# Kernel tuning notes

Hardware: AMD Instinct MI355X
Metric: run time of the kernel (lower is better)

## Reference

```python
import jax, jax.numpy as jnp
import numpy as np

B, T, L, D, H, S = 8, 8, 257, 1024, 16, 8
C = D // H


def _ln(x, g, b, axes):
    mu = jnp.mean(x, axes, keepdims=True)
    var = jnp.var(x, axes, keepdims=True)
    return (x - mu) * jax.lax.rsqrt(var + 1e-5) * g + b


def setup_inputs() -> dict:
    key = jax.random.key(0)
    ks = jax.random.split(key, 16)
    r = lambda i, shape, std=0.02: jax.random.normal(ks[i], shape, jnp.float32) * std
    return dict(
        x=r(0, (B, T, L, D), 1.0),
        s=r(1, (B, S, D), 1.0),
        te=r(2, (T, D), 1.0),
        patch_mask=jnp.zeros((B, T, 1, L - 1, 1), jnp.float32),
        in_proj_w=r(3, (3 * D, D)), in_proj_b=r(4, (3 * D,)),
        out_w=r(5, (D, D)), out_b=r(6, (D,)),
        ln1_g=jnp.ones(D), ln1_b=jnp.zeros(D),
        ln2_g=jnp.ones(D), ln2_b=jnp.zeros(D),
        fc_w=r(7, (4 * D, D)), fc_b=r(8, (4 * D,)),
        proj_w=r(9, (D, 4 * D)), proj_b=r(10, (D,)),
        smlp_ln_g=jnp.ones(D), smlp_ln_b=jnp.zeros(D),
        smlp_w1=r(11, (D // 8, D), 0.001), smlp_w2=r(12, (D, D // 8), 0.001),
        lnte_g=jnp.ones((T, D)), lnte_b=jnp.zeros((T, D)),
        conv_w=r(13, (D, 1, 3), 0.001), conv_b=jnp.zeros(D),
    )


def reference(x, s, te, patch_mask, in_proj_w, in_proj_b, out_w, out_b,
              ln1_g, ln1_b, ln2_g, ln2_b, fc_w, fc_b, proj_w, proj_b,
              smlp_ln_g, smlp_ln_b, smlp_w1, smlp_w2, lnte_g, lnte_b,
              conv_w, conv_b):
    scale = 1.0 / (C ** 0.5)

    def qkv(z):
        p = z @ in_proj_w.T + in_proj_b
        return jnp.split(p, 3, axis=-1)

    heads = lambda a: a.reshape(*a.shape[:-1], H, C)

    def mlp(z):
        h = z @ fc_w.T + fc_b
        h = h * jax.nn.sigmoid(1.702 * h)  # QuickGELU
        return h @ proj_w.T + proj_b

    # ---- spatial attention (per frame) ----
    xn = _ln(x, ln1_g, ln1_b, -1)
    q, k, v = [heads(a) for a in qkv(xn)]           # [B,T,L,H,C]
    aff = jnp.einsum('ntqhc,ntkhc->ntqkh', q * scale, k)
    aff = jax.nn.softmax(aff, axis=3)               # softmax over key dim (-2)
    mix = jnp.einsum('ntqlh,ntlhc->ntqhc', aff, v)
    out = mix.reshape(B, T, L, D) @ out_w.T + out_b

    # ---- syno-token branch ----
    s_mlp = (_ln(s, smlp_ln_g, smlp_ln_b, -1) @ smlp_w1.T) @ smlp_w2.T
    sn = _ln(s + s_mlp, ln1_g, ln1_b, -1)
    te_n = _ln(te, lnte_g, lnte_b, (-2, -1))        # LayerNorm over (frames, d)
    s_q, s_k, s_v = [heads(a) for a in qkv(sn)]     # [B,S,H,C]
    te_q, te_k, te_v = [a.reshape(T, 1, H, C) for a in qkv(te_n)]

    kk = k[:, :, 1:] + te_k                          # [B,T,L-1,H,C]
    vv = v[:, :, 1:] + te_v
    s_aff = jnp.einsum('nqhc,ntkhc->ntqkh', s_q * scale, kk) + patch_mask
    s_aff = jax.nn.softmax(s_aff, axis=3)
    s_mix = jnp.einsum('ntqlh,ntlhc->ntqhc', s_aff, vv)   # [B,T,S,H,C]

    # depthwise temporal conv over frames, with residual
    z = s_mix.transpose(0, 2, 3, 4, 1).reshape(B * S, D, T)   # [B*S, D, T]
    zc = jax.lax.conv_general_dilated(
        z, conv_w, window_strides=(1,), padding=[(1, 1)],
        dimension_numbers=('NCH', 'OIH', 'NCH'), feature_group_count=D)
    z = zc + conv_b[None, :, None] + z
    s_mix = z.reshape(B, S, H, C, T).transpose(0, 4, 1, 2, 3)  # [B,T,S,H,C]
    s_mix = s_mix.mean(axis=1)                                 # [B,S,H,C]
    s_out = s_mix.reshape(B, S, D) @ out_w.T + out_b

    # ---- residual + MLP ----
    x = x + out
    x = x + mlp(_ln(x, ln2_g, ln2_b, -1))
    s = s + s_out
    s = s + mlp(_ln(s, ln2_g, ln2_b, -1))
    return (x, s)
```

## Files before the change

kernel.cpp:

```cpp
#include <hip/hip_runtime.h>
#include <hip/hip_bf16.h>

#define BB 8
#define TT 8
#define LL 257
#define DD 1024
#define HH 16
#define CC 64
#define SS 8
#define NTOK (BB*TT*LL)
#define D3 (3*DD)
#define DFF (4*DD)
#define MMAIN 16384
#define MTAIL 64

typedef unsigned short u16;
typedef __attribute__((ext_vector_type(8))) short short8;
typedef __attribute__((ext_vector_type(4))) short short4v;
typedef __attribute__((ext_vector_type(4))) float f32x4;

__device__ __forceinline__ float us2f(u16 u) {
    return __uint_as_float(((unsigned int)u) << 16);
}
__device__ __forceinline__ u16 f2us(float f) {
    unsigned int u = __float_as_uint(f);
    unsigned int rb = ((u >> 16) & 1u) + 0x7fffu;
    return (u16)((u + rb) >> 16);
}

__device__ __forceinline__ void gload_lds16(const u16* g, u16* l) {
    __builtin_amdgcn_global_load_lds(
        (__attribute__((address_space(1))) void*)(void*)g,
        (__attribute__((address_space(3))) void*)(void*)l, 16, 0, 0);
}

__global__ __launch_bounds__(256)
void cvt_w(const float* __restrict__ in, u16* __restrict__ out, int n4)
{
    int i = blockIdx.x * 256 + threadIdx.x;
    if (i >= n4) return;
    float4 v = reinterpret_cast<const float4*>(in)[i];
    ushort4 o;
    o.x = f2us(v.x); o.y = f2us(v.y); o.z = f2us(v.z); o.w = f2us(v.w);
    reinterpret_cast<ushort4*>(out)[i] = o;
}

__global__ __launch_bounds__(256)
void ln_rows(const float* __restrict__ X, const float* __restrict__ R,
             const float* __restrict__ g, const float* __restrict__ bta,
             u16* __restrict__ out, int M)
{
    int row = blockIdx.x;
    if (row >= M) return;
    const float* x = X + (size_t)row * DD;
    const float* r = R ? R + (size_t)row * DD : nullptr;
    int t = threadIdx.x;
    float v[4]; float s1 = 0.f, s2 = 0.f;
#pragma unroll
    for (int i = 0; i < 4; ++i) {
        float val = x[t + 256 * i];
        if (r) val += r[t + 256 * i];
        v[i] = val; s1 += val; s2 += val * val;
    }
#pragma unroll
    for (int o = 32; o > 0; o >>= 1) { s1 += __shfl_xor(s1, o, 64); s2 += __shfl_xor(s2, o, 64); }
    __shared__ float red[10];
    int wid = t >> 6, lane = t & 63;
    if (lane == 0) { red[wid] = s1; red[4 + wid] = s2; }
    __syncthreads();
    if (t == 0) {
        float a = red[0] + red[1] + red[2] + red[3];
        float q = red[4] + red[5] + red[6] + red[7];
        float mu = a * (1.f / DD);
        float var = q * (1.f / DD) - mu * mu;
        red[8] = mu; red[9] = rsqrtf(var + 1e-5f);
    }
    __syncthreads();
    float mu = red[8], rs = red[9];
#pragma unroll
    for (int i = 0; i < 4; ++i) {
        int c = t + 256 * i;
        out[(size_t)row * DD + c] = f2us((v[i] - mu) * rs * g[c] + bta[c]);
    }
}

__global__ __launch_bounds__(256)
void s_prep(const float* __restrict__ s, const float* __restrict__ te,
            const float* __restrict__ smlp_g, const float* __restrict__ smlp_b,
            const float* __restrict__ ln1_g, const float* __restrict__ ln1_b,
            const float* __restrict__ lnte_g, const float* __restrict__ lnte_b,
            const u16* __restrict__ w1b, const u16* __restrict__ w2b,
            u16* __restrict__ snte)
{
    const int blk = blockIdx.x, t = threadIdx.x;
    __shared__ float red[10];
    const int wid = t >> 6, lane = t & 63;

    if (blk == 64) {
        const int NE = TT * DD;
        float s1 = 0.f, s2 = 0.f;
        for (int i = t; i < NE; i += 256) { float v = te[i]; s1 += v; s2 += v * v; }
#pragma unroll
        for (int o = 32; o > 0; o >>= 1) { s1 += __shfl_xor(s1, o, 64); s2 += __shfl_xor(s2, o, 64); }
        if (lane == 0) { red[wid] = s1; red[4 + wid] = s2; }
        __syncthreads();
        if (t == 0) {
            float a = red[0] + red[1] + red[2] + red[3];
            float q = red[4] + red[5] + red[6] + red[7];
            float mu = a / (float)NE;
            float var = q / (float)NE - mu * mu;
            red[8] = mu; red[9] = rsqrtf(var + 1e-5f);
        }
        __syncthreads();
        float mu = red[8], rs = red[9];
        for (int i = t; i < NE; i += 256)
            snte[(size_t)64 * DD + i] = f2us((te[i] - mu) * rs * lnte_g[i] + lnte_b[i]);
        return;
    }

    __shared__ float xrow[1024];
    __shared__ float h1[128];
    const float* sr = s + (size_t)blk * DD;

    float v[4]; float s1 = 0.f, s2 = 0.f;
#pragma unroll
    for (int i = 0; i < 4; ++i) {
        float val = sr[t + 256 * i];
        v[i] = val; s1 += val; s2 += val * val;
    }
#pragma unroll
    for (int o = 32; o > 0; o >>= 1) { s1 += __shfl_xor(s1, o, 64); s2 += __shfl_xor(s2, o, 64); }
    if (lane == 0) { red[wid] = s1; red[4 + wid] = s2; }
    __syncthreads();
    if (t == 0) {
        float a = red[0] + red[1] + red[2] + red[3];
        float q = red[4] + red[5] + red[6] + red[7];
        float mu = a * (1.f / DD);
        float var = q * (1.f / DD) - mu * mu;
        red[8] = mu; red[9] = rsqrtf(var + 1e-5f);
    }
    __syncthreads();
    {
        float mu = red[8], rs = red[9];
#pragma unroll
        for (int i = 0; i < 4; ++i) {
            int c = t + 256 * i;
            xrow[c] = (v[i] - mu) * rs * smlp_g[c] + smlp_b[c];
        }
    }
    __syncthreads();
    if (t < 128) {
        const u16* wr_ = w1b + (size_t)t * DD;
        float a0 = 0.f, a1 = 0.f;
        for (int k = 0; k < DD; k += 8) {
            short4v wa = *reinterpret_cast<const short4v*>(&wr_[k]);
            short4v wb = *reinterpret_cast<const short4v*>(&wr_[k + 4]);
#pragma unroll
            for (int j = 0; j < 4; ++j) {
                a0 += xrow[k + j] * us2f((u16)wa[j]);
                a1 += xrow[k + 4 + j] * us2f((u16)wb[j]);
            }
        }
        h1[t] = a0 + a1;
    }
    __syncthreads();
    float w[4]; s1 = 0.f; s2 = 0.f;
#pragma unroll
    for (int i = 0; i < 4; ++i) {
        int d = t + 256 * i;
        const u16* w2r = w2b + (size_t)d * 128;
        float a = 0.f;
        for (int k = 0; k < 128; k += 4) {
            short4v wa = *reinterpret_cast<const short4v*>(&w2r[k]);
#pragma unroll
            for (int j = 0; j < 4; ++j) a += h1[k + j] * us2f((u16)wa[j]);
        }
        float val = sr[d] + a;
        w[i] = val; s1 += val; s2 += val * val;
    }
#pragma unroll
    for (int o = 32; o > 0; o >>= 1) { s1 += __shfl_xor(s1, o, 64); s2 += __shfl_xor(s2, o, 64); }
    __syncthreads();
    if (lane == 0) { red[wid] = s1; red[4 + wid] = s2; }
    __syncthreads();
    if (t == 0) {
        float a = red[0] + red[1] + red[2] + red[3];
        float q = red[4] + red[5] + red[6] + red[7];
        float mu = a * (1.f / DD);
        float var = q * (1.f / DD) - mu * mu;
        red[8] = mu; red[9] = rsqrtf(var + 1e-5f);
    }
    __syncthreads();
    {
        float mu = red[8], rs = red[9];
#pragma unroll
        for (int i = 0; i < 4; ++i) {
            int d = t + 256 * i;
            snte[(size_t)blk * DD + d] = f2us((w[i] - mu) * rs * ln1_g[d] + ln1_b[d]);
        }
    }
}

enum { EPI_BF16 = 0, EPI_GELU = 1, EPI_RES = 2, EPI_F32 = 3 };

template<int EPI>
__global__ __launch_bounds__(512)
void gemm256(const u16* __restrict__ A, const u16* __restrict__ W,
             const float* __restrict__ bias, int M, int N, int K,
             u16* __restrict__ outB, float* __restrict__ outF,
             const float* __restrict__ res)
{
    __shared__ u16 lds[2][4][8192];
    const int tid = threadIdx.x;
    const int lane = tid & 63;
    const int wid = tid >> 6;
    const int wr = wid >> 2, wc = wid & 3;

    const int gx = gridDim.x;
    const int nwg = gx * gridDim.y;
    int bid = blockIdx.y * gx + blockIdx.x;
    int qq = nwg >> 3, rr = nwg & 7;
    int xcd = bid & 7, idx = bid >> 3;
    int nb = (xcd < rr ? xcd * (qq + 1) : rr * (qq + 1) + (xcd - rr) * qq) + idx;
    const int m0 = (nb / gx) * 256, n0 = (nb % gx) * 256;

    int u0 = tid, u1 = tid + 512;
    int g0 = u0 >> 6, kb0 = (u0 >> 4) & 3, r0 = u0 & 15;
    int g1 = u1 >> 6, kb1 = (u1 >> 4) & 3, r1 = u1 & 15;
    int ar0 = m0 + g0 * 16 + r0; if (ar0 >= M) ar0 = M - 1;
    int ar1 = m0 + g1 * 16 + r1; if (ar1 >= M) ar1 = M - 1;
    int br0 = n0 + g0 * 16 + r0;
    int br1 = n0 + g1 * 16 + r1;
    const u16* pa0 = A + (size_t)ar0 * K + kb0 * 8;
    const u16* pa1 = A + (size_t)ar1 * K + kb1 * 8;
    const u16* pb0 = W + (size_t)br0 * K + kb0 * 8;
    const u16* pb1 = W + (size_t)br1 * K + kb1 * 8;

    f32x4 acc[8][4];
#pragma unroll
    for (int i = 0; i < 8; ++i)
#pragma unroll
        for (int j = 0; j < 4; ++j)
            acc[i][j] = (f32x4){0.f, 0.f, 0.f, 0.f};

    auto stageA = [&](int kt, int s, int bf) {
        int kc = kt * 64 + s * 32;
        gload_lds16(pa0 + kc, &lds[bf][s * 2][u0 * 8]);
        gload_lds16(pa1 + kc, &lds[bf][s * 2][u1 * 8]);
    };
    auto stageB = [&](int kt, int s, int bf) {
        int kc = kt * 64 + s * 32;
        gload_lds16(pb0 + kc, &lds[bf][s * 2 + 1][u0 * 8]);
        gload_lds16(pb1 + kc, &lds[bf][s * 2 + 1][u1 * 8]);
    };

    const int nk = K >> 6;
    stageA(0, 0, 0); stageB(0, 0, 0); stageA(0, 1, 0); stageB(0, 1, 0);
    asm volatile("s_waitcnt vmcnt(4)" ::: "memory");
    __builtin_amdgcn_s_barrier();
    __builtin_amdgcn_sched_barrier(0);

    for (int t = 0; t < nk; ++t) {
        const int bf = t & 1, bn = bf ^ 1;
        const bool st = (t + 1 < nk);
        short8 aq[4], bq[4];
#pragma unroll
        for (int j = 0; j < 4; ++j)
            bq[j] = *reinterpret_cast<const short8*>(&lds[bf][1][(wc * 4 + j) * 512 + lane * 8]);
#pragma unroll
        for (int i = 0; i < 4; ++i)
            aq[i] = *reinterpret_cast<const short8*>(&lds[bf][0][(wr * 8 + i) * 512 + lane * 8]);
        if (st) stageA(t + 1, 0, bn);
        __builtin_amdgcn_s_barrier();
        __builtin_amdgcn_s_setprio(1);
#pragma unroll
        for (int i = 0; i < 4; ++i)
#pragma unroll
            for (int j = 0; j < 4; ++j)
                acc[i][j] = __builtin_amdgcn_mfma_f32_16x16x32_bf16(aq[i], bq[j], acc[i][j], 0, 0, 0);
        __builtin_amdgcn_s_setprio(0);
        __builtin_amdgcn_s_barrier();
        __builtin_amdgcn_sched_barrier(0);
#pragma unroll
        for (int i = 0; i < 4; ++i)
            aq[i] = *reinterpret_cast<const short8*>(&lds[bf][0][(wr * 8 + 4 + i) * 512 + lane * 8]);
        if (st) stageB(t + 1, 0, bn);
        __builtin_amdgcn_s_barrier();
        __builtin_amdgcn_s_setprio(1);
#pragma unroll
        for (int i = 0; i < 4; ++i)
#pragma unroll
            for (int j = 0; j < 4; ++j)
                acc[4 + i][j] = __builtin_amdgcn_mfma_f32_16x16x32_bf16(aq[i], bq[j], acc[4 + i][j], 0, 0, 0);
        __builtin_amdgcn_s_setprio(0);
        if (st) asm volatile("s_waitcnt vmcnt(4)" ::: "memory");
        else    asm volatile("s_waitcnt vmcnt(0)" ::: "memory");
        __builtin_amdgcn_s_barrier();
        __builtin_amdgcn_sched_barrier(0);
#pragma unroll
        for (int j = 0; j < 4; ++j)
            bq[j] = *reinterpret_cast<const short8*>(&lds[bf][3][(wc * 4 + j) * 512 + lane * 8]);
#pragma unroll
        for (int i = 0; i < 4; ++i)
            aq[i] = *reinterpret_cast<const short8*>(&lds[bf][2][(wr * 8 + i) * 512 + lane * 8]);
        if (st) stageA(t + 1, 1, bn);
        __builtin_amdgcn_s_barrier();
        __builtin_amdgcn_s_setprio(1);
#pragma unroll
        for (int i = 0; i < 4; ++i)
#pragma unroll
            for (int j = 0; j < 4; ++j)
                acc[i][j] = __builtin_amdgcn_mfma_f32_16x16x32_bf16(aq[i], bq[j], acc[i][j], 0, 0, 0);
        __builtin_amdgcn_s_setprio(0);
        __builtin_amdgcn_s_barrier();
        __builtin_amdgcn_sched_barrier(0);
#pragma unroll
        for (int i = 0; i < 4; ++i)
            aq[i] = *reinterpret_cast<const short8*>(&lds[bf][2][(wr * 8 + 4 + i) * 512 + lane * 8]);
        if (st) stageB(t + 1, 1, bn);
        __builtin_amdgcn_s_barrier();
        __builtin_amdgcn_s_setprio(1);
#pragma unroll
        for (int i = 0; i < 4; ++i)
#pragma unroll
            for (int j = 0; j < 4; ++j)
                acc[4 + i][j] = __builtin_amdgcn_mfma_f32_16x16x32_bf16(aq[i], bq[j], acc[4 + i][j], 0, 0, 0);
        __builtin_amdgcn_s_setprio(0);
        if (st) asm volatile("s_waitcnt vmcnt(4)" ::: "memory");
        __builtin_amdgcn_s_barrier();
        __builtin_amdgcn_sched_barrier(0);
    }

    const int cn = lane & 15, cr = (lane >> 4) * 4;
#pragma unroll
    for (int i = 0; i < 8; ++i) {
#pragma unroll
        for (int r = 0; r < 4; ++r) {
            int m = m0 + wr * 128 + i * 16 + cr + r;
            if (m >= M) continue;
#pragma unroll
            for (int j = 0; j < 4; ++j) {
                int n = n0 + wc * 64 + j * 16 + cn;
                float c = acc[i][j][r];
                if (bias) c += bias[n];
                size_t o = (size_t)m * N + n;
                if (EPI == EPI_BF16) outB[o] = f2us(c);
                else if (EPI == EPI_GELU) { float gg = c / (1.f + __expf(-1.702f * c)); outB[o] = f2us(gg); }
                else if (EPI == EPI_RES) outF[o] = res[o] + c;
                else outF[o] = c;
            }
        }
    }
}

template<int EPI>
__global__ __launch_bounds__(256)
void gemm_mfma(const u16* __restrict__ A, const u16* __restrict__ W,
               const float* __restrict__ bias, int M, int N, int K,
               u16* __restrict__ outB, float* __restrict__ outF,
               const float* __restrict__ res)
{
    __shared__ u16 Als[3][128 * 32];
    __shared__ u16 Bls[3][128 * 32];
    const int tid = threadIdx.x;
    const int lane = tid & 63;
    const int wid = tid >> 6;
    const int wm = (wid >> 1) * 64, wn = (wid & 1) * 64;

    const int gx = gridDim.x;
    const int nwg = gx * gridDim.y;
    int bid = blockIdx.y * gx + blockIdx.x;
    int qq = nwg >> 3, rr = nwg & 7;
    int xcd = bid & 7, idx = bid >> 3;
    int nb = (xcd < rr ? xcd * (qq + 1) : rr * (qq + 1) + (xcd - rr) * qq) + idx;
    const int m0 = (nb / gx) * 128, n0 = (nb % gx) * 128;

    int o0 = tid, o1 = tid + 256;
    int g0 = o0 >> 6, kb0 = (o0 >> 4) & 3, r0 = o0 & 15;
    int g1 = o1 >> 6, kb1 = (o1 >> 4) & 3, r1 = o1 & 15;
    int ar0 = m0 + g0 * 16 + r0; if (ar0 >= M) ar0 = M - 1;
    int ar1 = m0 + g1 * 16 + r1; if (ar1 >= M) ar1 = M - 1;
    int br0 = n0 + g0 * 16 + r0;
    int br1 = n0 + g1 * 16 + r1;
    const u16* a0 = A + (size_t)ar0 * K + kb0 * 8;
    const u16* a1 = A + (size_t)ar1 * K + kb1 * 8;
    const u16* b0 = W + (size_t)br0 * K + kb0 * 8;
    const u16* b1 = W + (size_t)br1 * K + kb1 * 8;

    f32x4 acc[4][4];
#pragma unroll
    for (int i = 0; i < 4; ++i)
#pragma unroll
        for (int j = 0; j < 4; ++j)
            acc[i][j] = (f32x4){0.f, 0.f, 0.f, 0.f};

    auto stage = [&](int kt, int sl) {
        int kk = kt << 5;
        gload_lds16(a0 + kk, &Als[sl][o0 * 8]);
        gload_lds16(a1 + kk, &Als[sl][o1 * 8]);
        gload_lds16(b0 + kk, &Bls[sl][o0 * 8]);
        gload_lds16(b1 + kk, &Bls[sl][o1 * 8]);
    };
    auto compute = [&](int sl) {
        short8 af[4], bfr[4];
#pragma unroll
        for (int i = 0; i < 4; ++i)
            af[i] = *reinterpret_cast<const short8*>(&Als[sl][((wm >> 4) + i) * 512 + lane * 8]);
#pragma unroll
        for (int j = 0; j < 4; ++j)
            bfr[j] = *reinterpret_cast<const short8*>(&Bls[sl][((wn >> 4) + j) * 512 + lane * 8]);
        __builtin_amdgcn_s_setprio(1);
#pragma unroll
        for (int i = 0; i < 4; ++i)
#pragma unroll
            for (int j = 0; j < 4; ++j)
                acc[i][j] = __builtin_amdgcn_mfma_f32_16x16x32_bf16(af[i], bfr[j], acc[i][j], 0, 0, 0);
        __builtin_amdgcn_s_setprio(0);
    };

    const int nk = K >> 5;
    stage(0, 0);
    stage(1, 1);
    asm volatile("s_waitcnt vmcnt(4)" ::: "memory");
    __builtin_amdgcn_s_barrier();
    __builtin_amdgcn_sched_barrier(0);

    int t = 0;
    for (; t < nk - 2; ++t) {
        stage(t + 2, (t + 2) % 3);
        compute(t % 3);
        asm volatile("s_waitcnt vmcnt(4)" ::: "memory");
        __builtin_amdgcn_s_barrier();
        __builtin_amdgcn_sched_barrier(0);
    }
    compute(t % 3);
    asm volatile("s_waitcnt vmcnt(0)" ::: "memory");
    __builtin_amdgcn_s_barrier();
    __builtin_amdgcn_sched_barrier(0);
    ++t;
    compute(t % 3);

    const int cn = lane & 15, cr = (lane >> 4) * 4;
#pragma unroll
    for (int i = 0; i < 4; ++i) {
#pragma unroll
        for (int r = 0; r < 4; ++r) {
            int m = m0 + wm + i * 16 + cr + r;
            if (m >= M) continue;
#pragma unroll
            for (int j = 0; j < 4; ++j) {
                int n = n0 + wn + j * 16 + cn;
                float c = acc[i][j][r];
                if (bias) c += bias[n];
                size_t o = (size_t)m * N + n;
                if (EPI == EPI_BF16) outB[o] = f2us(c);
                else if (EPI == EPI_GELU) { float gg = c / (1.f + __expf(-1.702f * c)); outB[o] = f2us(gg); }
                else if (EPI == EPI_RES) outF[o] = res[o] + c;
                else outF[o] = c;
            }
        }
    }
}

#define KSTR 72
#define VSTR 296
#define PSTR 40

__global__ __launch_bounds__(256)
void spatial_attn(const u16* __restrict__ qkv, u16* __restrict__ mix)
{
    const int h = blockIdx.x, bt = blockIdx.y;
    const int hoff = h * CC;
    const size_t base = (size_t)bt * LL * D3;
    __shared__ u16 Kls[257 * KSTR];
    __shared__ u16 Vt[64 * VSTR];
    __shared__ u16 Pb[4][16 * PSTR];
    const int tid = threadIdx.x, lane = tid & 63, w = tid >> 6;
    const int c15 = lane & 15, g = lane >> 4;

    for (int idx = tid; idx < 257 * 8; idx += 256) {
        int row = idx >> 3, c8 = (idx & 7) << 3;
        float4 v = *reinterpret_cast<const float4*>(&qkv[base + (size_t)row * D3 + DD + hoff + c8]);
        *reinterpret_cast<float4*>(&Kls[row * KSTR + c8]) = v;
    }
    for (int idx = tid; idx < 288 * 64; idx += 256) {
        int key = idx >> 6, c = idx & 63;
        u16 v = 0;
        if (key < 257) v = qkv[base + (size_t)key * D3 + 2 * DD + hoff + c];
        Vt[c * VSTR + key] = v;
    }
    __syncthreads();

    u16* pb = Pb[w];
    for (int qt = w; qt < 17; qt += 4) {
        int qrow = qt * 16 + c15; if (qrow > 256) qrow = 256;
        const u16* qp = &qkv[base + (size_t)qrow * D3 + hoff + g * 8];
        short8 a0 = *reinterpret_cast<const short8*>(qp);
        short8 a1 = *reinterpret_cast<const short8*>(qp + 32);

        f32x4 sc[17];
#pragma unroll
        for (int t = 0; t < 17; ++t) sc[t] = (f32x4){0.f, 0.f, 0.f, 0.f};
        __builtin_amdgcn_s_setprio(1);
#pragma unroll
        for (int t = 0; t < 17; ++t) {
            int krow = t * 16 + c15; if (krow > 256) krow = 256;
            short8 b0 = *reinterpret_cast<const short8*>(&Kls[krow * KSTR + g * 8]);
            short8 b1 = *reinterpret_cast<const short8*>(&Kls[krow * KSTR + 32 + g * 8]);
            sc[t] = __builtin_amdgcn_mfma_f32_16x16x32_bf16(a0, b0, sc[t], 0, 0, 0);
            sc[t] = __builtin_amdgcn_mfma_f32_16x16x32_bf16(a1, b1, sc[t], 0, 0, 0);
        }
        __builtin_amdgcn_s_setprio(0);

        const bool lastv = (c15 == 0);
#pragma unroll
        for (int r = 0; r < 4; ++r) {
            float mx = -1e30f;
#pragma unroll
            for (int t = 0; t < 17; ++t) {
                float v = sc[t][r] * 0.125f;
                if (t == 16 && !lastv) v = -1e30f;
                sc[t][r] = v;
                mx = fmaxf(mx, v);
            }
            mx = fmaxf(mx, __shfl_xor(mx, 1, 64));
            mx = fmaxf(mx, __shfl_xor(mx, 2, 64));
            mx = fmaxf(mx, __shfl_xor(mx, 4, 64));
            mx = fmaxf(mx, __shfl_xor(mx, 8, 64));
            float sum = 0.f;
#pragma unroll
            for (int t = 0; t < 17; ++t) { float e = __expf(sc[t][r] - mx); sc[t][r] = e; sum += e; }
            sum += __shfl_xor(sum, 1, 64);
            sum += __shfl_xor(sum, 2, 64);
            sum += __shfl_xor(sum, 4, 64);
            sum += __shfl_xor(sum, 8, 64);
            float is = 1.f / sum;
#pragma unroll
            for (int t = 0; t < 17; ++t) sc[t][r] *= is;
        }

        f32x4 oacc[4];
#pragma unroll
        for (int ct = 0; ct < 4; ++ct) oacc[ct] = (f32x4){0.f, 0.f, 0.f, 0.f};
#pragma unroll
        for (int k0 = 0; k0 < 9; ++k0) {
            const int t0 = 2 * k0, t1 = 2 * k0 + 1;
#pragma unroll
            for (int r = 0; r < 4; ++r) {
                pb[(4 * g + r) * PSTR + c15]      = f2us(sc[t0][r]);
                pb[(4 * g + r) * PSTR + 16 + c15] = (t1 < 17) ? f2us(sc[t1][r]) : (u16)0;
            }
            short8 pa = *reinterpret_cast<const short8*>(&pb[c15 * PSTR + 8 * g]);
            __builtin_amdgcn_s_setprio(1);
#pragma unroll
            for (int ct = 0; ct < 4; ++ct) {
                short8 vb = *reinterpret_cast<const short8*>(&Vt[(16 * ct + c15) * VSTR + 32 * k0 + 8 * g]);
                oacc[ct] = __builtin_amdgcn_mfma_f32_16x16x32_bf16(pa, vb, oacc[ct], 0, 0, 0);
            }
            __builtin_amdgcn_s_setprio(0);
        }

#pragma unroll
        for (int r = 0; r < 4; ++r) {
            int q = qt * 16 + 4 * g + r;
            if (q >= LL) continue;
            size_t ob = ((size_t)bt * LL + q) * DD + hoff;
#pragma unroll
            for (int ct = 0; ct < 4; ++ct)
                mix[ob + 16 * ct + c15] = f2us(oacc[ct][r]);
        }
    }
}

#define SK 68

__global__ __launch_bounds__(256)
void s_attn(const u16* __restrict__ qkv, const u16* __restrict__ snqkv,
            const u16* __restrict__ teqkv, const float* __restrict__ pmask,
            float* __restrict__ smix)
{
    const int h = blockIdx.x, bt = blockIdx.y, b = bt >> 3, t = bt & 7;
    const int hoff = h * CC;
    const int tid = threadIdx.x, lane = tid & 63, w = tid >> 6;
    __shared__ u16 Kls[256 * SK];
    __shared__ u16 Vls[256 * SK];
    __shared__ float pls[4][256];
    const size_t base = (size_t)bt * LL * D3;

    const int c8 = (tid & 7) * 8;
    const u16* tekp = &teqkv[t * D3 + DD + hoff + c8];
    const u16* tevp = &teqkv[t * D3 + 2 * DD + hoff + c8];
    float tek[8], tev[8];
#pragma unroll
    for (int j = 0; j < 8; ++j) { tek[j] = us2f(tekp[j]); tev[j] = us2f(tevp[j]); }
#pragma unroll
    for (int pass = 0; pass < 8; ++pass) {
        int key = (tid >> 3) + 32 * pass;
        const u16* kp = &qkv[base + (size_t)(key + 1) * D3 + DD + hoff + c8];
        const u16* vp = &qkv[base + (size_t)(key + 1) * D3 + 2 * DD + hoff + c8];
        short4v k0 = *reinterpret_cast<const short4v*>(kp);
        short4v k1 = *reinterpret_cast<const short4v*>(kp + 4);
        short4v v0 = *reinterpret_cast<const short4v*>(vp);
        short4v v1 = *reinterpret_cast<const short4v*>(vp + 4);
        short4v ok0, ok1, ov0, ov1;
#pragma unroll
        for (int j = 0; j < 4; ++j) {
            ok0[j] = (short)f2us(us2f((u16)k0[j]) + tek[j]);
            ok1[j] = (short)f2us(us2f((u16)k1[j]) + tek[4 + j]);
            ov0[j] = (short)f2us(us2f((u16)v0[j]) + tev[j]);
            ov1[j] = (short)f2us(us2f((u16)v1[j]) + tev[4 + j]);
        }
        *reinterpret_cast<short4v*>(&Kls[key * SK + c8]) = ok0;
        *reinterpret_cast<short4v*>(&Kls[key * SK + c8 + 4]) = ok1;
        *reinterpret_cast<short4v*>(&Vls[key * SK + c8]) = ov0;
        *reinterpret_cast<short4v*>(&Vls[key * SK + c8 + 4]) = ov1;
    }
    __syncthreads();

    const float* pm = pmask + (size_t)bt * 256;
    for (int qi = w; qi < SS; qi += 4) {
        float qc = us2f(snqkv[(size_t)(b * SS + qi) * D3 + hoff + lane]) * 0.125f;
        float sc[4] = {0.f, 0.f, 0.f, 0.f};
        for (int c = 0; c < CC; ++c) {
            float qv = __shfl(qc, c, 64);
#pragma unroll
            for (int j = 0; j < 4; ++j)
                sc[j] += qv * us2f(Kls[(lane + 64 * j) * SK + c]);
        }
#pragma unroll
        for (int j = 0; j < 4; ++j) sc[j] += pm[lane + 64 * j];
        float mx = fmaxf(fmaxf(sc[0], sc[1]), fmaxf(sc[2], sc[3]));
#pragma unroll
        for (int o = 32; o > 0; o >>= 1) mx = fmaxf(mx, __shfl_xor(mx, o, 64));
        float sum = 0.f;
#pragma unroll
        for (int j = 0; j < 4; ++j) { sc[j] = __expf(sc[j] - mx); sum += sc[j]; }
#pragma unroll
        for (int o = 32; o > 0; o >>= 1) sum += __shfl_xor(sum, o, 64);
        float inv = 1.f / sum;
#pragma unroll
        for (int j = 0; j < 4; ++j) pls[w][lane + 64 * j] = sc[j] * inv;
        float acc = 0.f;
        for (int key = 0; key < 256; ++key)
            acc += pls[w][key] * us2f(Vls[key * SK + lane]);
        smix[(((size_t)bt * SS + qi) * HH + h) * CC + lane] = acc;
    }
}

__global__ __launch_bounds__(256)
void conv_mean(const float* __restrict__ smix, const float* __restrict__ cw,
               const float* __restrict__ cb, u16* __restrict__ out)
{
    int idx = blockIdx.x * 256 + threadIdx.x;
    int d = idx & 1023;
    int bs = idx >> 10;
    int b = bs >> 3, s_ = bs & 7;
    float z[TT];
#pragma unroll
    for (int t = 0; t < TT; ++t)
        z[t] = smix[((size_t)(b * TT + t) * SS + s_) * DD + d];
    float w0 = cw[d * 3], w1 = cw[d * 3 + 1], w2 = cw[d * 3 + 2];
    float acc = 0.f;
#pragma unroll
    for (int t = 0; t < TT; ++t) {
        float zc = w1 * z[t];
        if (t > 0)      zc += w0 * z[t - 1];
        if (t < TT - 1) zc += w2 * z[t + 1];
        acc += z[t] + zc;
    }
    out[(size_t)bs * DD + d] = f2us(acc * 0.125f + cb[d]);
}

extern "C" void kernel_launch(void* const* d_in, const int* in_sizes, int n_in,
                              void* d_out, int out_size, void* d_ws, size_t ws_size,
                              hipStream_t stream)
{
    const float* x      = (const float*)d_in[0];
    const float* s      = (const float*)d_in[1];
    const float* te     = (const float*)d_in[2];
    const float* pmask  = (const float*)d_in[3];
    const float* in_w   = (const float*)d_in[4];
    const float* in_b   = (const float*)d_in[5];
    const float* out_w  = (const float*)d_in[6];
    const float* out_b  = (const float*)d_in[7];
    const float* ln1_g  = (const float*)d_in[8];
    const float* ln1_b  = (const float*)d_in[9];
    const float* ln2_g  = (const float*)d_in[10];
    const float* ln2_b  = (const float*)d_in[11];
    const float* fc_w   = (const float*)d_in[12];
    const float* fc_b   = (const float*)d_in[13];
    const float* proj_w = (const float*)d_in[14];
    const float* proj_b = (const float*)d_in[15];
    const float* smlp_g = (const float*)d_in[16];
    const float* smlp_b = (const float*)d_in[17];
    const float* w1     = (const float*)d_in[18];
    const float* w2     = (const float*)d_in[19];
    const float* lnte_g = (const float*)d_in[20];
    const float* lnte_b = (const float*)d_in[21];
    const float* conv_w = (const float*)d_in[22];
    const float* conv_b = (const float*)d_in[23];

    float* outx = (float*)d_out;
    float* outs = outx + (size_t)NTOK * DD;

    char* ws = (char*)d_ws;
    u16* qkv    = (u16*)ws;
    u16* mixb   = (u16*)(ws + (size_t)NTOK * D3 * 2);
    u16* hidden = qkv;
    u16* xn     = (u16*)(ws + (size_t)NTOK * DFF * 2);
    char* sm    = ws + (size_t)NTOK * DFF * 2 + (size_t)NTOK * DD * 2;
    u16*  snte   = (u16*)sm;  sm += (size_t)72 * DD * 2;
    u16*  sqkv72 = (u16*)sm;  sm += (size_t)72 * D3 * 2;
    float* smix = (float*)sm; sm += (size_t)BB * TT * SS * DD * 4;
    u16*  smm   = (u16*)sm;   sm += 64 * DD * 2;
    u16*  ln2s  = (u16*)sm;   sm += 64 * DD * 2;
    u16*  hids  = (u16*)sm;   sm += 64 * DFF * 2;
    u16* in_wb   = (u16*)sm;  sm += (size_t)D3 * DD * 2;
    u16* out_wb  = (u16*)sm;  sm += (size_t)DD * DD * 2;
    u16* fc_wb   = (u16*)sm;  sm += (size_t)DFF * DD * 2;
    u16* proj_wb = (u16*)sm;  sm += (size_t)DD * DFF * 2;
    u16* w1b     = (u16*)sm;  sm += (size_t)128 * DD * 2;
    u16* w2b     = (u16*)sm;  sm += (size_t)DD * 128 * 2;

    const float* FNULL = nullptr;
    u16* UNULL = nullptr;

    auto cvt = [&](const float* src, u16* dst, int n) {
        hipLaunchKernelGGL(cvt_w, dim3((n / 4 + 255) / 256), dim3(256), 0, stream, src, dst, n / 4);
    };
    cvt(in_w,   in_wb,   D3 * DD);
    cvt(out_w,  out_wb,  DD * DD);
    cvt(fc_w,   fc_wb,   DFF * DD);
    cvt(proj_w, proj_wb, DD * DFF);
    cvt(w1,     w1b,     128 * DD);
    cvt(w2,     w2b,     DD * 128);

    const int MT64 = MMAIN / 256;

    hipLaunchKernelGGL(ln_rows, dim3(NTOK), dim3(256), 0, stream, x, FNULL, ln1_g, ln1_b, xn, NTOK);
    hipLaunchKernelGGL((gemm256<EPI_BF16>), dim3(D3 / 256, MT64), dim3(512), 0, stream,
                       xn, in_wb, in_b, MMAIN, D3, DD, qkv, (float*)nullptr, FNULL);
    hipLaunchKernelGGL((gemm_mfma<EPI_BF16>), dim3(D3 / 128, 1), dim3(256), 0, stream,
                       xn + (size_t)MMAIN * DD, in_wb, in_b, MTAIL, D3, DD,
                       qkv + (size_t)MMAIN * D3, (float*)nullptr, FNULL);
    hipLaunchKernelGGL(spatial_attn, dim3(HH, BB * TT), dim3(256), 0, stream, qkv, mixb);
    hipLaunchKernelGGL((gemm256<EPI_RES>), dim3(DD / 256, MT64), dim3(512), 0, stream,
                       mixb, out_wb, out_b, MMAIN, DD, DD, UNULL, outx, x);
    hipLaunchKernelGGL((gemm_mfma<EPI_RES>), dim3(DD / 128, 1), dim3(256), 0, stream,
                       mixb + (size_t)MMAIN * DD, out_wb, out_b, MTAIL, DD, DD,
                       UNULL, outx + (size_t)MMAIN * DD, x + (size_t)MMAIN * DD);
    hipLaunchKernelGGL(s_prep, dim3(65), dim3(256), 0, stream,
                       s, te, smlp_g, smlp_b, ln1_g, ln1_b, lnte_g, lnte_b, w1b, w2b, snte);
    hipLaunchKernelGGL((gemm_mfma<EPI_BF16>), dim3(D3 / 128, 1), dim3(256), 0, stream,
                       snte, in_wb, in_b, 72, D3, DD, sqkv72, (float*)nullptr, FNULL);
    hipLaunchKernelGGL(s_attn, dim3(HH, BB * TT), dim3(256), 0, stream,
                       qkv, sqkv72, sqkv72 + (size_t)64 * D3, pmask, smix);
    hipLaunchKernelGGL(conv_mean, dim3(256), dim3(256), 0, stream, smix, conv_w, conv_b, smm);
    hipLaunchKernelGGL((gemm_mfma<EPI_RES>), dim3(DD / 128, 1), dim3(256), 0, stream,
                       smm, out_wb, out_b, 64, DD, DD, UNULL, outs, s);
    hipLaunchKernelGGL(ln_rows, dim3(NTOK), dim3(256), 0, stream, outx, FNULL, ln2_g, ln2_b, xn, NTOK);
    hipLaunchKernelGGL((gemm256<EPI_GELU>), dim3(DFF / 256, MT64), dim3(512), 0, stream,
                       xn, fc_wb, fc_b, MMAIN, DFF, DD, hidden, (float*)nullptr, FNULL);
    hipLaunchKernelGGL((gemm_mfma<EPI_GELU>), dim3(DFF / 128, 1), dim3(256), 0, stream,
                       xn + (size_t)MMAIN * DD, fc_wb, fc_b, MTAIL, DFF, DD,
                       hidden + (size_t)MMAIN * DFF, (float*)nullptr, FNULL);
    hipLaunchKernelGGL((gemm256<EPI_RES>), dim3(DD / 256, MT64), dim3(512), 0, stream,
                       hidden, proj_wb, proj_b, MMAIN, DD, DFF, UNULL, outx, outx);
    hipLaunchKernelGGL((gemm_mfma<EPI_RES>), dim3(DD / 128, 1), dim3(256), 0, stream,
                       hidden + (size_t)MMAIN * DFF, proj_wb, proj_b, MTAIL, DD, DFF,
                       UNULL, outx + (size_t)MMAIN * DD, outx + (size_t)MMAIN * DD);
    hipLaunchKernelGGL(ln_rows, dim3(64), dim3(256), 0, stream, outs, FNULL, ln2_g, ln2_b, ln2s, 64);
    hipLaunchKernelGGL((gemm_mfma<EPI_GELU>), dim3(DFF / 128, 1), dim3(256), 0, stream,
                       ln2s, fc_wb, fc_b, 64, DFF, DD, hids, (float*)nullptr, FNULL);
    hipLaunchKernelGGL((gemm_mfma<EPI_RES>), dim3(DD / 128, 1), dim3(256), 0, stream,
                       hids, proj_wb, proj_b, 64, DD, DFF, UNULL, outs, outs);
}
```

Measured before the change: 1.426 ms.

## Replace 256x256 GEMM plus tail kernel with single 128x128 GEMM kernel

The 512-thread 256x256-tile GEMM and the separate 3-stage 128x128 tail GEMM are replaced by one 256-thread 128x128-tile kernel derived from the large one. Every projection now runs as a single launch covering all rows, which drops the tail launches. The smaller tile halves per-block reuse of A and W loads and raises global and LDS traffic per flop. In exchange it uses less LDS per block, so more blocks can be resident. The vmcnt(4) waits were kept while each k-step now issues both A and B loads together, so the wait accounting may be wrong.

```diff
diff --git a/kernel.cpp b/kernel.cpp
--- a/kernel.cpp
+++ b/kernel.cpp
@@ -11,8 +11,6 @@
 #define NTOK (BB*TT*LL)
 #define D3 (3*DD)
 #define DFF (4*DD)
-#define MMAIN 16384
-#define MTAIL 64
 
 typedef unsigned short u16;
 typedef __attribute__((ext_vector_type(8))) short short8;
@@ -204,17 +202,17 @@
 enum { EPI_BF16 = 0, EPI_GELU = 1, EPI_RES = 2, EPI_F32 = 3 };
 
 template<int EPI>
-__global__ __launch_bounds__(512)
-void gemm256(const u16* __restrict__ A, const u16* __restrict__ W,
+__global__ __launch_bounds__(256)
+void gemm128(const u16* __restrict__ A, const u16* __restrict__ W,
              const float* __restrict__ bias, int M, int N, int K,
              u16* __restrict__ outB, float* __restrict__ outF,
              const float* __restrict__ res)
 {
-    __shared__ u16 lds[2][4][8192];
+    __shared__ u16 lds[2][4][4096];
     const int tid = threadIdx.x;
     const int lane = tid & 63;
     const int wid = tid >> 6;
-    const int wr = wid >> 2, wc = wid & 3;
+    const int wr = wid >> 1, wc = wid & 1;
 
     const int gx = gridDim.x;
     const int nwg = gx * gridDim.y;
@@ -222,9 +220,9 @@
     int qq = nwg >> 3, rr = nwg & 7;
     int xcd = bid & 7, idx = bid >> 3;
     int nb = (xcd < rr ? xcd * (qq + 1) : rr * (qq + 1) + (xcd - rr) * qq) + idx;
-    const int m0 = (nb / gx) * 256, n0 = (nb % gx) * 256;
-
-    int u0 = tid, u1 = tid + 512;
+    const int m0 = (nb / gx) * 128, n0 = (nb % gx) * 128;
+
+    int u0 = tid, u1 = tid + 256;
     int g0 = u0 >> 6, kb0 = (u0 >> 4) & 3, r0 = u0 & 15;
     int g1 = u1 >> 6, kb1 = (u1 >> 4) & 3, r1 = u1 & 15;
     int ar0 = m0 + g0 * 16 + r0; if (ar0 >= M) ar0 = M - 1;
@@ -236,9 +234,9 @@
     const u16* pb0 = W + (size_t)br0 * K + kb0 * 8;
     const u16* pb1 = W + (size_t)br1 * K + kb1 * 8;
 
-    f32x4 acc[8][4];
-#pragma unroll
-    for (int i = 0; i < 8; ++i)
+    f32x4 acc[4][4];
+#pragma unroll
+    for (int i = 0; i < 4; ++i)
 #pragma unroll
         for (int j = 0; j < 4; ++j)
             acc[i][j] = (f32x4){0.f, 0.f, 0.f, 0.f};
@@ -266,11 +264,11 @@
         short8 aq[4], bq[4];
 #pragma unroll
         for (int j = 0; j < 4; ++j)
-            bq[j] = *reinterpret_cast<const short8*>(&lds[bf][1][(wc * 4 + j) * 512 + lane * 8]);
+            bq[j] = *reinterpret_cast<const short8*>(&lds[bf][1][((wc * 4 + j) * 64 + lane) * 8]);
 #pragma unroll
         for (int i = 0; i < 4; ++i)
-            aq[i] = *reinterpret_cast<const short8*>(&lds[bf][0][(wr * 8 + i) * 512 + lane * 8]);
-        if (st) stageA(t + 1, 0, bn);
+            aq[i] = *reinterpret_cast<const short8*>(&lds[bf][0][((wr * 4 + i) * 64 + lane) * 8]);
+        if (st) { stageA(t + 1, 0, bn); stageB(t + 1, 0, bn); }
         __builtin_amdgcn_s_barrier();
         __builtin_amdgcn_s_setprio(1);
 #pragma unroll
@@ -278,20 +276,6 @@
 #pragma unroll
             for (int j = 0; j < 4; ++j)
                 acc[i][j] = __builtin_amdgcn_mfma_f32_16x16x32_bf16(aq[i], bq[j], acc[i][j], 0, 0, 0);
-        __builtin_amdgcn_s_setprio(0);
-        __builtin_amdgcn_s_barrier();
-        __builtin_amdgcn_sched_barrier(0);
-#pragma unroll
-        for (int i = 0; i < 4; ++i)
-            aq[i] = *reinterpret_cast<const short8*>(&lds[bf][0][(wr * 8 + 4 + i) * 512 + lane * 8]);
-        if (st) stageB(t + 1, 0, bn);
-        __builtin_amdgcn_s_barrier();
-        __builtin_amdgcn_s_setprio(1);
-#pragma unroll
-        for (int i = 0; i < 4; ++i)
-#pragma unroll
-            for (int j = 0; j < 4; ++j)
-                acc[4 + i][j] = __builtin_amdgcn_mfma_f32_16x16x32_bf16(aq[i], bq[j], acc[4 + i][j], 0, 0, 0);
         __builtin_amdgcn_s_setprio(0);
         if (st) asm volatile("s_waitcnt vmcnt(4)" ::: "memory");
         else    asm volatile("s_waitcnt vmcnt(0)" ::: "memory");
@@ -299,11 +283,11 @@
         __builtin_amdgcn_sched_barrier(0);
 #pragma unroll
         for (int j = 0; j < 4; ++j)
-            bq[j] = *reinterpret_cast<const short8*>(&lds[bf][3][(wc * 4 + j) * 512 + lane * 8]);
+            bq[j] = *reinterpret_cast<const short8*>(&lds[bf][3][((wc * 4 + j) * 64 + lane) * 8]);
 #pragma unroll
         for (int i = 0; i < 4; ++i)
-            aq[i] = *reinterpret_cast<const short8*>(&lds[bf][2][(wr * 8 + i) * 512 + lane * 8]);
-        if (st) stageA(t + 1, 1, bn);
+            aq[i] = *reinterpret_cast<const short8*>(&lds[bf][2][((wr * 4 + i) * 64 + lane) * 8]);
+        if (st) { stageA(t + 1, 1, bn); stageB(t + 1, 1, bn); }
         __builtin_amdgcn_s_barrier();
         __builtin_amdgcn_s_setprio(1);
 #pragma unroll
@@ -311,20 +295,6 @@
 #pragma unroll
             for (int j = 0; j < 4; ++j)
                 acc[i][j] = __builtin_amdgcn_mfma_f32_16x16x32_bf16(aq[i], bq[j], acc[i][j], 0, 0, 0);
-        __builtin_amdgcn_s_setprio(0);
-        __builtin_amdgcn_s_barrier();
-        __builtin_amdgcn_sched_barrier(0);
-#pragma unroll
-        for (int i = 0; i < 4; ++i)
-            aq[i] = *reinterpret_cast<const short8*>(&lds[bf][2][(wr * 8 + 4 + i) * 512 + lane * 8]);
-        if (st) stageB(t + 1, 1, bn);
-        __builtin_amdgcn_s_barrier();
-        __builtin_amdgcn_s_setprio(1);
-#pragma unroll
-        for (int i = 0; i < 4; ++i)
-#pragma unroll
-            for (int j = 0; j < 4; ++j)
-                acc[4 + i][j] = __builtin_amdgcn_mfma_f32_16x16x32_bf16(aq[i], bq[j], acc[4 + i][j], 0, 0, 0);
         __builtin_amdgcn_s_setprio(0);
         if (st) asm volatile("s_waitcnt vmcnt(4)" ::: "memory");
         __builtin_amdgcn_s_barrier();
@@ -333,123 +303,14 @@
 
     const int cn = lane & 15, cr = (lane >> 4) * 4;
 #pragma unroll
-    for (int i = 0; i < 8; ++i) {
+    for (int i = 0; i < 4; ++i) {
 #pragma unroll
         for (int r = 0; r < 4; ++r) {
-            int m = m0 + wr * 128 + i * 16 + cr + r;
+            int m = m0 + wr * 64 + i * 16 + cr + r;
             if (m >= M) continue;
 #pragma unroll
             for (int j = 0; j < 4; ++j) {
                 int n = n0 + wc * 64 + j * 16 + cn;
-                float c = acc[i][j][r];
-                if (bias) c += bias[n];
-                size_t o = (size_t)m * N + n;
-                if (EPI == EPI_BF16) outB[o] = f2us(c);
-                else if (EPI == EPI_GELU) { float gg = c / (1.f + __expf(-1.702f * c)); outB[o] = f2us(gg); }
-                else if (EPI == EPI_RES) outF[o] = res[o] + c;
-                else outF[o] = c;
-            }
-        }
-    }
-}
-
-template<int EPI>
-__global__ __launch_bounds__(256)
-void gemm_mfma(const u16* __restrict__ A, const u16* __restrict__ W,
-               const float* __restrict__ bias, int M, int N, int K,
-               u16* __restrict__ outB, float* __restrict__ outF,
-               const float* __restrict__ res)
-{
-    __shared__ u16 Als[3][128 * 32];
-    __shared__ u16 Bls[3][128 * 32];
-    const int tid = threadIdx.x;
-    const int lane = tid & 63;
-    const int wid = tid >> 6;
-    const int wm = (wid >> 1) * 64, wn = (wid & 1) * 64;
-
-    const int gx = gridDim.x;
-    const int nwg = gx * gridDim.y;
-    int bid = blockIdx.y * gx + blockIdx.x;
-    int qq = nwg >> 3, rr = nwg & 7;
-    int xcd = bid & 7, idx = bid >> 3;
-    int nb = (xcd < rr ? xcd * (qq + 1) : rr * (qq + 1) + (xcd - rr) * qq) + idx;
-    const int m0 = (nb / gx) * 128, n0 = (nb % gx) * 128;
-
-    int o0 = tid, o1 = tid + 256;
-    int g0 = o0 >> 6, kb0 = (o0 >> 4) & 3, r0 = o0 & 15;
-    int g1 = o1 >> 6, kb1 = (o1 >> 4) & 3, r1 = o1 & 15;
-    int ar0 = m0 + g0 * 16 + r0; if (ar0 >= M) ar0 = M - 1;
-    int ar1 = m0 + g1 * 16 + r1; if (ar1 >= M) ar1 = M - 1;
-    int br0 = n0 + g0 * 16 + r0;
-    int br1 = n0 + g1 * 16 + r1;
-    const u16* a0 = A + (size_t)ar0 * K + kb0 * 8;
-    const u16* a1 = A + (size_t)ar1 * K + kb1 * 8;
-    const u16* b0 = W + (size_t)br0 * K + kb0 * 8;
-    const u16* b1 = W + (size_t)br1 * K + kb1 * 8;
-
-    f32x4 acc[4][4];
-#pragma unroll
-    for (int i = 0; i < 4; ++i)
-#pragma unroll
-        for (int j = 0; j < 4; ++j)
-            acc[i][j] = (f32x4){0.f, 0.f, 0.f, 0.f};
-
-    auto stage = [&](int kt, int sl) {
-        int kk = kt << 5;
-        gload_lds16(a0 + kk, &Als[sl][o0 * 8]);
-        gload_lds16(a1 + kk, &Als[sl][o1 * 8]);
-        gload_lds16(b0 + kk, &Bls[sl][o0 * 8]);
-        gload_lds16(b1 + kk, &Bls[sl][o1 * 8]);
-    };
-    auto compute = [&](int sl) {
-        short8 af[4], bfr[4];
-#pragma unroll
-        for (int i = 0; i < 4; ++i)
-            af[i] = *reinterpret_cast<const short8*>(&Als[sl][((wm >> 4) + i) * 512 + lane * 8]);
-#pragma unroll
-        for (int j = 0; j < 4; ++j)
-            bfr[j] = *reinterpret_cast<const short8*>(&Bls[sl][((wn >> 4) + j) * 512 + lane * 8]);
-        __builtin_amdgcn_s_setprio(1);
-#pragma unroll
-        for (int i = 0; i < 4; ++i)
-#pragma unroll
-            for (int j = 0; j < 4; ++j)
-                acc[i][j] = __builtin_amdgcn_mfma_f32_16x16x32_bf16(af[i], bfr[j], acc[i][j], 0, 0, 0);
-        __builtin_amdgcn_s_setprio(0);
-    };
-
-    const int nk = K >> 5;
-    stage(0, 0);
-    stage(1, 1);
-    asm volatile("s_waitcnt vmcnt(4)" ::: "memory");
-    __builtin_amdgcn_s_barrier();
-    __builtin_amdgcn_sched_barrier(0);
-
-    int t = 0;
-    for (; t < nk - 2; ++t) {
-        stage(t + 2, (t + 2) % 3);
-        compute(t % 3);
-        asm volatile("s_waitcnt vmcnt(4)" ::: "memory");
-        __builtin_amdgcn_s_barrier();
-        __builtin_amdgcn_sched_barrier(0);
-    }
-    compute(t % 3);
-    asm volatile("s_waitcnt vmcnt(0)" ::: "memory");
-    __builtin_amdgcn_s_barrier();
-    __builtin_amdgcn_sched_barrier(0);
-    ++t;
-    compute(t % 3);
-
-    const int cn = lane & 15, cr = (lane >> 4) * 4;
-#pragma unroll
-    for (int i = 0; i < 4; ++i) {
-#pragma unroll
-        for (int r = 0; r < 4; ++r) {
-            int m = m0 + wm + i * 16 + cr + r;
-            if (m >= M) continue;
-#pragma unroll
-            for (int j = 0; j < 4; ++j) {
-                int n = n0 + wn + j * 16 + cn;
                 float c = acc[i][j][r];
                 if (bias) c += bias[n];
                 size_t o = (size_t)m * N + n;
@@ -735,43 +596,31 @@
     cvt(w1,     w1b,     128 * DD);
     cvt(w2,     w2b,     DD * 128);
 
-    const int MT64 = MMAIN / 256;
+    const int MT = (NTOK + 127) / 128;
 
     hipLaunchKernelGGL(ln_rows, dim3(NTOK), dim3(256), 0, stream, x, FNULL, ln1_g, ln1_b, xn, NTOK);
-    hipLaunchKernelGGL((gemm256<EPI_BF16>), dim3(D3 / 256, MT64), dim3(512), 0, stream,
-                       xn, in_wb, in_b, MMAIN, D3, DD, qkv, (float*)nullptr, FNULL);
-    hipLaunchKernelGGL((gemm_mfma<EPI_BF16>), dim3(D3 / 128, 1), dim3(256), 0, stream,
-                       xn + (size_t)MMAIN * DD, in_wb, in_b, MTAIL, D3, DD,
-                       qkv + (size_t)MMAIN * D3, (float*)nullptr, FNULL);
+    hipLaunchKernelGGL((gemm128<EPI_BF16>), dim3(D3 / 128, MT), dim3(256), 0, stream,
+                       xn, in_wb, in_b, NTOK, D3, DD, qkv, (float*)nullptr, FNULL);
     hipLaunchKernelGGL(spatial_attn, dim3(HH, BB * TT), dim3(256), 0, stream, qkv, mixb);
-    hipLaunchKernelGGL((gemm256<EPI_RES>), dim3(DD / 256, MT64), dim3(512), 0, stream,
-                       mixb, out_wb, out_b, MMAIN, DD, DD, UNULL, outx, x);
-    hipLaunchKernelGGL((gemm_mfma<EPI_RES>), dim3(DD / 128, 1), dim3(256), 0, stream,
-                       mixb + (size_t)MMAIN * DD, out_wb, out_b, MTAIL, DD, DD,
-                       UNULL, outx + (size_t)MMAIN * DD, x + (size_t)MMAIN * DD);
+    hipLaunchKernelGGL((gemm128<EPI_RES>), dim3(DD / 128, MT), dim3(256), 0, stream,
+                       mixb, out_wb, out_b, NTOK, DD, DD, UNULL, outx, x);
     hipLaunchKernelGGL(s_prep, dim3(65), dim3(256), 0, stream,
                        s, te, smlp_g, smlp_b, ln1_g, ln1_b, lnte_g, lnte_b, w1b, w2b, snte);
-    hipLaunchKernelGGL((gemm_mfma<EPI_BF16>), dim3(D3 / 128, 1), dim3(256), 0, stream,
+    hipLaunchKernelGGL((gemm128<EPI_BF16>), dim3(D3 / 128, 1), dim3(256), 0, stream,
                        snte, in_wb, in_b, 72, D3, DD, sqkv72, (float*)nullptr, FNULL);
     hipLaunchKernelGGL(s_attn, dim3(HH, BB * TT), dim3(256), 0, stream,
                        qkv, sqkv72, sqkv72 + (size_t)64 * D3, pmask, smix);
     hipLaunchKernelGGL(conv_mean, dim3(256), dim3(256), 0, stream, smix, conv_w, conv_b, smm);
-    hipLaunchKernelGGL((gemm_mfma<EPI_RES>), dim3(DD / 128, 1), dim3(256), 0, stream,
+    hipLaunchKernelGGL((gemm128<EPI_RES>), dim3(DD / 128, 1), dim3(256), 0, stream,
                        smm, out_wb, out_b, 64, DD, DD, UNULL, outs, s);
     hipLaunchKernelGGL(ln_rows, dim3(NTOK), dim3(256), 0, stream, outx, FNULL, ln2_g, ln2_b, xn, NTOK);
-    hipLaunchKernelGGL((gemm256<EPI_GELU>), dim3(DFF / 256, MT64), dim3(512), 0, stream,
-                       xn, fc_wb, fc_b, MMAIN, DFF, DD, hidden, (float*)nullptr, FNULL);
-    hipLaunchKernelGGL((gemm_mfma<EPI_GELU>), dim3(DFF / 128, 1), dim3(256), 0, stream,
-                       xn + (size_t)MMAIN * DD, fc_wb, fc_b, MTAIL, DFF, DD,
-                       hidden + (size_t)MMAIN * DFF, (float*)nullptr, FNULL);
-    hipLaunchKernelGGL((gemm256<EPI_RES>), dim3(DD / 256, MT64), dim3(512), 0, stream,
-                       hidden, proj_wb, proj_b, MMAIN, DD, DFF, UNULL, outx, outx);
-    hipLaunchKernelGGL((gemm_mfma<EPI_RES>), dim3(DD / 128, 1), dim3(256), 0, stream,
-                       hidden + (size_t)MMAIN * DFF, proj_wb, proj_b, MTAIL, DD, DFF,
-                       UNULL, outx + (size_t)MMAIN * DD, outx + (size_t)MMAIN * DD);
+    hipLaunchKernelGGL((gemm128<EPI_GELU>), dim3(DFF / 128, MT), dim3(256), 0, stream,
+                       xn, fc_wb, fc_b, NTOK, DFF, DD, hidden, (float*)nullptr, FNULL);
+    hipLaunchKernelGGL((gemm128<EPI_RES>), dim3(DD / 128, MT), dim3(256), 0, stream,
+                       hidden, proj_wb, proj_b, NTOK, DD, DFF, UNULL, outx, outx);
     hipLaunchKernelGGL(ln_rows, dim3(64), dim3(256), 0, stream, outs, FNULL, ln2_g, ln2_b, ln2s, 64);
-    hipLaunchKernelGGL((gemm_mfma<EPI_GELU>), dim3(DFF / 128, 1), dim3(256), 0, stream,
+    hipLaunchKernelGGL((gemm128<EPI_GELU>), dim3(DFF / 128, 1), dim3(256), 0, stream,
                        ln2s, fc_wb, fc_b, 64, DFF, DD, hids, (float*)nullptr, FNULL);
-    hipLaunchKernelGGL((gemm_mfma<EPI_RES>), dim3(DD / 128, 1), dim3(256), 0, stream,
+    hipLaunchKernelGGL((gemm128<EPI_RES>), dim3(DD / 128, 1), dim3(256), 0, stream,
                        hids, proj_wb, proj_b, 64, DD, DFF, UNULL, outs, outs);
 }
```

Result: slower. 1.493 ms (+4.7%).

## Simplify GEMM main loop to one barrier per K-tile with whole-tile prefetch

Applied to the files above, without the earlier changes.

Replaces the four-phase ping-pong schedule, which has many barriers and staggered A/B half-tile loads, with a simpler loop. Each iteration issues all eight global-to-LDS loads for the next K tile up front, then runs two sub-steps each loading 8 A and 4 B fragments and doing 32 MFMAs, and ends with a full vmcnt(0) wait and a single barrier. The goal is to cut barrier and synchronisation overhead. In exchange it loses the fine-grained interleaving of memory and compute, and it raises register pressure because 8 A fragments are held at once.

```diff
diff --git a/kernel.cpp b/kernel.cpp
--- a/kernel.cpp
+++ b/kernel.cpp
@@ -243,90 +243,45 @@
         for (int j = 0; j < 4; ++j)
             acc[i][j] = (f32x4){0.f, 0.f, 0.f, 0.f};
 
-    auto stageA = [&](int kt, int s, int bf) {
-        int kc = kt * 64 + s * 32;
-        gload_lds16(pa0 + kc, &lds[bf][s * 2][u0 * 8]);
-        gload_lds16(pa1 + kc, &lds[bf][s * 2][u1 * 8]);
+    auto stage = [&](int kt, int bf) {
+        int kc = kt << 6;
+        gload_lds16(pa0 + kc,      &lds[bf][0][u0 * 8]);
+        gload_lds16(pa1 + kc,      &lds[bf][0][u1 * 8]);
+        gload_lds16(pb0 + kc,      &lds[bf][1][u0 * 8]);
+        gload_lds16(pb1 + kc,      &lds[bf][1][u1 * 8]);
+        gload_lds16(pa0 + kc + 32, &lds[bf][2][u0 * 8]);
+        gload_lds16(pa1 + kc + 32, &lds[bf][2][u1 * 8]);
+        gload_lds16(pb0 + kc + 32, &lds[bf][3][u0 * 8]);
+        gload_lds16(pb1 + kc + 32, &lds[bf][3][u1 * 8]);
     };
-    auto stageB = [&](int kt, int s, int bf) {
-        int kc = kt * 64 + s * 32;
-        gload_lds16(pb0 + kc, &lds[bf][s * 2 + 1][u0 * 8]);
-        gload_lds16(pb1 + kc, &lds[bf][s * 2 + 1][u1 * 8]);
-    };
 
     const int nk = K >> 6;
-    stageA(0, 0, 0); stageB(0, 0, 0); stageA(0, 1, 0); stageB(0, 1, 0);
-    asm volatile("s_waitcnt vmcnt(4)" ::: "memory");
+    stage(0, 0);
+    asm volatile("s_waitcnt vmcnt(0)" ::: "memory");
     __builtin_amdgcn_s_barrier();
     __builtin_amdgcn_sched_barrier(0);
 
     for (int t = 0; t < nk; ++t) {
         const int bf = t & 1, bn = bf ^ 1;
-        const bool st = (t + 1 < nk);
-        short8 aq[4], bq[4];
-#pragma unroll
-        for (int j = 0; j < 4; ++j)
-            bq[j] = *reinterpret_cast<const short8*>(&lds[bf][1][(wc * 4 + j) * 512 + lane * 8]);
-#pragma unroll
-        for (int i = 0; i < 4; ++i)
-            aq[i] = *reinterpret_cast<const short8*>(&lds[bf][0][(wr * 8 + i) * 512 + lane * 8]);
-        if (st) stageA(t + 1, 0, bn);
-        __builtin_amdgcn_s_barrier();
-        __builtin_amdgcn_s_setprio(1);
-#pragma unroll
-        for (int i = 0; i < 4; ++i)
+        if (t + 1 < nk) stage(t + 1, bn);
+#pragma unroll
+        for (int ks = 0; ks < 2; ++ks) {
+            short8 aq[8], bq[4];
 #pragma unroll
             for (int j = 0; j < 4; ++j)
-                acc[i][j] = __builtin_amdgcn_mfma_f32_16x16x32_bf16(aq[i], bq[j], acc[i][j], 0, 0, 0);
-        __builtin_amdgcn_s_setprio(0);
-        __builtin_amdgcn_s_barrier();
-        __builtin_amdgcn_sched_barrier(0);
-#pragma unroll
-        for (int i = 0; i < 4; ++i)
-            aq[i] = *reinterpret_cast<const short8*>(&lds[bf][0][(wr * 8 + 4 + i) * 512 + lane * 8]);
-        if (st) stageB(t + 1, 0, bn);
-        __builtin_amdgcn_s_barrier();
-        __builtin_amdgcn_s_setprio(1);
-#pragma unroll
-        for (int i = 0; i < 4; ++i)
-#pragma unroll
-            for (int j = 0; j < 4; ++j)
-                acc[4 + i][j] = __builtin_amdgcn_mfma_f32_16x16x32_bf16(aq[i], bq[j], acc[4 + i][j], 0, 0, 0);
-        __builtin_amdgcn_s_setprio(0);
-        if (st) asm volatile("s_waitcnt vmcnt(4)" ::: "memory");
-        else    asm volatile("s_waitcnt vmcnt(0)" ::: "memory");
-        __builtin_amdgcn_s_barrier();
-        __builtin_amdgcn_sched_barrier(0);
-#pragma unroll
-        for (int j = 0; j < 4; ++j)
-            bq[j] = *reinterpret_cast<const short8*>(&lds[bf][3][(wc * 4 + j) * 512 + lane * 8]);
-#pragma unroll
-        for (int i = 0; i < 4; ++i)
-            aq[i] = *reinterpret_cast<const short8*>(&lds[bf][2][(wr * 8 + i) * 512 + lane * 8]);
-        if (st) stageA(t + 1, 1, bn);
-        __builtin_amdgcn_s_barrier();
-        __builtin_amdgcn_s_setprio(1);
-#pragma unroll
-        for (int i = 0; i < 4; ++i)
-#pragma unroll
-            for (int j = 0; j < 4; ++j)
-                acc[i][j] = __builtin_amdgcn_mfma_f32_16x16x32_bf16(aq[i], bq[j], acc[i][j], 0, 0, 0);
-        __builtin_amdgcn_s_setprio(0);
-        __builtin_amdgcn_s_barrier();
-        __builtin_amdgcn_sched_barrier(0);
-#pragma unroll
-        for (int i = 0; i < 4; ++i)
-            aq[i] = *reinterpret_cast<const short8*>(&lds[bf][2][(wr * 8 + 4 + i) * 512 + lane * 8]);
-        if (st) stageB(t + 1, 1, bn);
-        __builtin_amdgcn_s_barrier();
-        __builtin_amdgcn_s_setprio(1);
-#pragma unroll
-        for (int i = 0; i < 4; ++i)
-#pragma unroll
-            for (int j = 0; j < 4; ++j)
-                acc[4 + i][j] = __builtin_amdgcn_mfma_f32_16x16x32_bf16(aq[i], bq[j], acc[4 + i][j], 0, 0, 0);
-        __builtin_amdgcn_s_setprio(0);
-        if (st) asm volatile("s_waitcnt vmcnt(4)" ::: "memory");
+                bq[j] = *reinterpret_cast<const short8*>(&lds[bf][ks * 2 + 1][(wc * 4 + j) * 512 + lane * 8]);
+#pragma unroll
+            for (int i = 0; i < 8; ++i)
+                aq[i] = *reinterpret_cast<const short8*>(&lds[bf][ks * 2][(wr * 8 + i) * 512 + lane * 8]);
+            __builtin_amdgcn_s_setprio(1);
+#pragma unroll
+            for (int i = 0; i < 8; ++i)
+#pragma unroll
+                for (int j = 0; j < 4; ++j)
+                    acc[i][j] = __builtin_amdgcn_mfma_f32_16x16x32_bf16(aq[i], bq[j], acc[i][j], 0, 0, 0);
+            __builtin_amdgcn_s_setprio(0);
+        }
+        asm volatile("s_waitcnt vmcnt(0)" ::: "memory");
         __builtin_amdgcn_s_barrier();
         __builtin_amdgcn_sched_barrier(0);
     }
```

Result: slower. 1.468 ms (+2.9%).
